# Optimization experiments

Measured on AMD Instinct MI355X. Metric: run time of the kernel, lower is better.

The kernel has to match this reference:

```python
import jax, jax.numpy as jnp
import numpy as np

B_, T_, N_ = 32, 96, 68
IN_F, HID, GRU_H, NCLS = 3, 128, 128, 10
DEG = 8
N_NODES = B_ * T_ * N_
N_EDGES = N_NODES * DEG


def setup_inputs() -> dict:
    key = jax.random.key(0)
    ks = jax.random.split(key, 16)
    s = 0.05
    rn = lambda k, shp: (jax.random.normal(k, shp, jnp.float32) * s)
    return {
        "x": jax.random.normal(ks[0], (N_NODES, IN_F), jnp.float32),
        "edge_index": jax.random.randint(ks[1], (2, N_EDGES), 0, N_NODES, jnp.int32),
        "W_gcn0": rn(ks[2], (IN_F, HID)),
        "b_gcn0": jnp.zeros((HID,), jnp.float32),
        "W_gcn1": rn(ks[3], (HID, HID)),
        "b_gcn1": jnp.zeros((HID,), jnp.float32),
        "W_mlp": rn(ks[4], (HID, HID)),
        "b_mlp": jnp.zeros((HID,), jnp.float32),
        "W_ih": rn(ks[5], (3 * GRU_H, HID)),
        "W_hh": rn(ks[6], (3 * GRU_H, GRU_H)),
        "b_ih": jnp.zeros((3 * GRU_H,), jnp.float32),
        "b_hh": jnp.zeros((3 * GRU_H,), jnp.float32),
        "W_c1": rn(ks[7], (GRU_H, GRU_H // 2)),
        "b_c1": jnp.zeros((GRU_H // 2,), jnp.float32),
        "W_c2": rn(ks[8], (GRU_H // 2, NCLS)),
        "b_c2": jnp.zeros((NCLS,), jnp.float32),
        "B": B_, "T": T_, "N": N_,
    }


def reference(x, edge_index, W_gcn0, b_gcn0, W_gcn1, b_gcn1, W_mlp, b_mlp,
              W_ih, W_hh, b_ih, b_hh, W_c1, b_c1, W_c2, b_c2, B, T, N):
    n_nodes = x.shape[0]
    src, dst = edge_index[0], edge_index[1]
    # GCN degree with self-loops: deg[i] = 1 + in-degree(i)
    deg = jnp.ones((n_nodes,), x.dtype).at[dst].add(1.0)
    d_isqrt = jax.lax.rsqrt(deg)
    self_norm = (d_isqrt * d_isqrt)[:, None]  # self-loop norm = 1/deg
    edge_norm = (d_isqrt[src] * d_isqrt[dst])[:, None]

    def gcn(h, W, b):
        h = h @ W
        agg = jax.ops.segment_sum(h[src] * edge_norm, dst, num_segments=n_nodes)
        return agg + h * self_norm + b

    h = jax.nn.relu(gcn(x, W_gcn0, b_gcn0))
    h = jax.nn.relu(gcn(h, W_gcn1, b_gcn1))
    h = jax.nn.relu(h @ W_mlp + b_mlp)  # node_mlp (dropout off in eval)

    frames = h.reshape(B, T, N, -1).mean(axis=2)  # [B, T, HID] frame pooling

    def gru_step(hs, xt):
        gi = xt @ W_ih.T + b_ih
        gh = hs @ W_hh.T + b_hh
        ir, iz, inn = jnp.split(gi, 3, axis=-1)
        hr, hz, hn = jnp.split(gh, 3, axis=-1)
        r = jax.nn.sigmoid(ir + hr)
        z = jax.nn.sigmoid(iz + hz)
        n_new = jnp.tanh(inn + r * hn)
        return (1.0 - z) * n_new + z * hs, None

    h0 = jnp.zeros((B, GRU_H), frames.dtype)
    hT, _ = jax.lax.scan(gru_step, h0, jnp.swapaxes(frames, 0, 1))

    hidden = jax.nn.relu(hT @ W_c1 + b_c1)
    return hidden @ W_c2 + b_c2  # logits [B, num_classes]
```

## Files before the change

### kernel.cpp

```cpp
#include <hip/hip_runtime.h>

#define NN_TOT 208896
#define E_TOT  1671168
#define B_SZ   32
#define T_SZ   96
#define NPF    68
#define HID    128
#define NBINS  204
#define CAP    9216
#define NSB    816

typedef _Float16 f16x8 __attribute__((ext_vector_type(8)));
typedef _Float16 f16x2v __attribute__((ext_vector_type(2)));
typedef float f32x4 __attribute__((ext_vector_type(4)));

__global__ __launch_bounds__(256) void k_scatter(const int* __restrict__ src, const int* __restrict__ dst,
                                                 int* __restrict__ gcur, int* __restrict__ er_tmp,
                                                 const float* __restrict__ Wih, const float* __restrict__ Whh,
                                                 const float* __restrict__ W1, const float* __restrict__ Wm,
                                                 const float* __restrict__ W0, const float* __restrict__ b0,
                                                 _Float16* __restrict__ Wihh, _Float16* __restrict__ Wihl,
                                                 _Float16* __restrict__ W1p, _Float16* __restrict__ Wmp,
                                                 _Float16* __restrict__ Whhp, _Float16* __restrict__ W0h,
                                                 _Float16* __restrict__ b0h) {
    const int bid = blockIdx.x;
    const int tid = threadIdx.x;
    if (bid >= NSB) {
        int i = (bid - NSB) * 256 + tid;
        {
            int e = i & 7;
            int lane = (i >> 3) & 63;
            int f = i >> 9;
            int j = f >> 2, kk = f & 3;
            int q = lane >> 4, p = lane & 15;
            float wv = Wih[(size_t)(j * 16 + p) * 128 + kk * 32 + q * 8 + e];
            _Float16 hi = (_Float16)wv;
            Wihh[i] = hi;
            Wihl[i] = (_Float16)(wv - (float)hi);
        }
        {
            int e = i & 7;
            int lane = (i >> 3) & 63;
            int f = i >> 9;
            int kk = f & 3, g = (f >> 2) % 3, wv = f / 12;
            int q = lane >> 4, c = lane & 15;
            Whhp[i] = (_Float16)Whh[(size_t)(g * 128 + 16 * wv + c) * 128 + kk * 32 + q * 8 + e];
        }
        if (i < 16384) {
            int f = i >> 9;
            int j = f >> 2, kk = f & 3;
            int lane = (i >> 3) & 63;
            int e = i & 7;
            int q = lane >> 4, p = lane & 15;
            int k = kk * 32 + q * 8 + e, n = j * 16 + p;
            W1p[i] = (_Float16)W1[k * 128 + n];
            Wmp[i] = (_Float16)Wm[k * 128 + n];
        }
        if (i < 384) W0h[i] = (_Float16)W0[i];
        if (i < 128) b0h[i] = (_Float16)b0[i];
        return;
    }
    __shared__ int hist[NBINS];
    __shared__ int lbase[NBINS];
    for (int i = tid; i < NBINS; i += 256) hist[i] = 0;
    __syncthreads();
    const int be = bid * 2048 + tid * 8;
    int s[8], d[8], rk[8];
    *(int4*)&s[0] = *(const int4*)&src[be];
    *(int4*)&s[4] = *(const int4*)&src[be + 4];
    *(int4*)&d[0] = *(const int4*)&dst[be];
    *(int4*)&d[4] = *(const int4*)&dst[be + 4];
#pragma unroll
    for (int j = 0; j < 8; ++j) rk[j] = atomicAdd(&hist[d[j] >> 10], 1);
    __syncthreads();
    for (int i = tid; i < NBINS; i += 256) lbase[i] = atomicAdd(&gcur[i], hist[i]);
    __syncthreads();
#pragma unroll
    for (int j = 0; j < 8; ++j) {
        int b = d[j] >> 10;
        er_tmp[(size_t)b * CAP + lbase[b] + rk[j]] = s[j] | ((d[j] & 1023) << 18);
    }
}

__global__ __launch_bounds__(256) void k_binsort2(const int* __restrict__ er_tmp, const int* __restrict__ gcur,
                                                  const float* __restrict__ x, int* __restrict__ er,
                                                  int2* __restrict__ row2, float4* __restrict__ xd) {
    __shared__ int lcnt[1024];
    __shared__ int lofs[1024];
    __shared__ int ts[256];
    const int tid = threadIdx.x;
    const int nb = blockIdx.x << 10;
    const int base0 = blockIdx.x * CAP;
    for (int i = tid; i < 1024; i += 256) lcnt[i] = 0;
    __syncthreads();
    const int nrec = gcur[blockIdx.x];
    int rec[36];
#pragma unroll
    for (int j = 0; j < 36; ++j) {
        int idx = tid + j * 256;
        rec[j] = (idx < nrec) ? er_tmp[base0 + idx] : -1;
    }
#pragma unroll
    for (int j = 0; j < 36; ++j)
        if (rec[j] >= 0) atomicAdd(&lcnt[rec[j] >> 18], 1);
    __syncthreads();
    const int base = tid * 4;
    const int c0 = lcnt[base], c1 = lcnt[base + 1], c2 = lcnt[base + 2], c3 = lcnt[base + 3];
    int ssum = c0 + c1 + c2 + c3;
    ts[tid] = ssum;
    __syncthreads();
    int inc = ssum;
    for (int off = 1; off < 256; off <<= 1) {
        int add = (tid >= off) ? ts[tid - off] : 0;
        __syncthreads();
        inc += add;
        ts[tid] = inc;
        __syncthreads();
    }
    const int b0 = base0 + (inc - ssum);
    lofs[base] = b0;
    lofs[base + 1] = b0 + c0;
    lofs[base + 2] = b0 + c0 + c1;
    lofs[base + 3] = b0 + c0 + c1 + c2;
    row2[nb + base] = make_int2(b0, b0 + c0);
    row2[nb + base + 1] = make_int2(b0 + c0, b0 + c0 + c1);
    row2[nb + base + 2] = make_int2(b0 + c0 + c1, b0 + c0 + c1 + c2);
    row2[nb + base + 3] = make_int2(b0 + c0 + c1 + c2, b0 + ssum);
    {
        const float4* xv = (const float4*)(x + 3 * (size_t)(nb + base));
        float4 a = xv[0], b = xv[1], c = xv[2];
        float i0 = 1.0f / sqrtf(1.f + (float)c0);
        float i1 = 1.0f / sqrtf(1.f + (float)c1);
        float i2 = 1.0f / sqrtf(1.f + (float)c2);
        float i3 = 1.0f / sqrtf(1.f + (float)c3);
        xd[nb + base + 0] = make_float4(a.x * i0, a.y * i0, a.z * i0, i0);
        xd[nb + base + 1] = make_float4(a.w * i1, b.x * i1, b.y * i1, i1);
        xd[nb + base + 2] = make_float4(b.z * i2, b.w * i2, c.x * i2, i2);
        xd[nb + base + 3] = make_float4(c.y * i3, c.z * i3, c.w * i3, i3);
    }
    __syncthreads();
#pragma unroll
    for (int j = 0; j < 36; ++j)
        if (rec[j] >= 0) {
            int p = atomicAdd(&lofs[rec[j] >> 18], 1);
            er[p] = rec[j] & 0x3FFFF;
        }
}

__global__ __launch_bounds__(256) void k_z0(const float4* __restrict__ xd, const int2* __restrict__ row2,
                                            const int* __restrict__ er, float4* __restrict__ z0out) {
    const int tid = threadIdx.x;
    const int blk = blockIdx.x;
    const int li = tid >> 2;
    const int slot = tid & 3;
    const int n = blk * 64 + li;
    const int2 be2 = row2[n];
    float p0 = 0.f, p1 = 0.f, p2 = 0.f;
    for (int ei = be2.x + slot; ei < be2.y; ei += 4) {
        float4 f = xd[er[ei]];
        p0 += f.x;
        p1 += f.y;
        p2 += f.z;
    }
    p0 += __shfl_xor(p0, 1); p1 += __shfl_xor(p1, 1); p2 += __shfl_xor(p2, 1);
    p0 += __shfl_xor(p0, 2); p1 += __shfl_xor(p1, 2); p2 += __shfl_xor(p2, 2);
    if (slot == 0) {
        const float4 own = xd[n];
        const float w = own.w;
        float4 z;
        z.x = w * (p0 + own.x);
        z.y = w * (p1 + own.y);
        z.z = w * (p2 + own.z);
        z.w = w;
        z0out[n] = z;
    }
}

__global__ __launch_bounds__(256, 4) void k_agg_mm(const float4* __restrict__ z0, const int2* __restrict__ row2,
                                                   const int* __restrict__ er, const _Float16* __restrict__ W0h,
                                                   const _Float16* __restrict__ b0h, const _Float16* __restrict__ W1p,
                                                   const float* __restrict__ b1, _Float16* __restrict__ h1) {
    __shared__ __align__(16) _Float16 As[64 * 136];
    const int tid = threadIdx.x;
    const int w = tid >> 6, lane = tid & 63;
    const int blk = blockIdx.x;

    {
        const int node = blk * 64 + lane;
        const int2 be2 = row2[node];
        const int beg = be2.x, end = be2.y;
        const f16x2v* __restrict__ W0p = (const f16x2v*)W0h;
        const f16x2v* __restrict__ b0p = (const f16x2v*)b0h;
        const int pb = w * 16;
        const f16x2v zero2 = {(_Float16)0.f, (_Float16)0.f};
        f16x2v w0p[16], w1p[16], w2p[16], bbp[16];
#pragma unroll
        for (int j = 0; j < 16; ++j) {
            w0p[j] = W0p[pb + j];
            w1p[j] = W0p[64 + pb + j];
            w2p[j] = W0p[128 + pb + j];
            bbp[j] = b0p[pb + j];
        }
        const float4 zs = z0[node];
        const _Float16 isd = (_Float16)zs.w;
        const f16x2v dnn = {isd, isd};
        f16x2v accp[16];
        {
            _Float16 sx = (_Float16)zs.x, sy = (_Float16)zs.y, sz = (_Float16)zs.z;
            f16x2v zxx = {sx, sx}, zyy = {sy, sy}, zzz = {sz, sz};
#pragma unroll
            for (int j = 0; j < 16; ++j) {
                f16x2v t = zxx * w0p[j] + (zyy * w1p[j] + (zzz * w2p[j] + bbp[j]));
                t = __builtin_elementwise_max(t, zero2);
                accp[j] = t * dnn;
            }
        }
        int ei = beg;
        for (; ei + 2 <= end; ei += 2) {
            int sa = er[ei], sb = er[ei + 1];
            float4 za = z0[sa];
            float4 zb = z0[sb];
            _Float16 ax = (_Float16)za.x, ay = (_Float16)za.y, az = (_Float16)za.z;
            _Float16 aen = (_Float16)za.w;
            _Float16 bx = (_Float16)zb.x, by = (_Float16)zb.y, bz = (_Float16)zb.z;
            _Float16 ben = (_Float16)zb.w;
            f16x2v axx = {ax, ax}, ayy = {ay, ay}, azz = {az, az}, aee = {aen, aen};
            f16x2v bxx = {bx, bx}, byy = {by, by}, bzz = {bz, bz}, bee = {ben, ben};
#pragma unroll
            for (int j = 0; j < 16; ++j) {
                f16x2v t = axx * w0p[j] + (ayy * w1p[j] + (azz * w2p[j] + bbp[j]));
                t = __builtin_elementwise_max(t, zero2);
                accp[j] = t * aee + accp[j];
            }
#pragma unroll
            for (int j = 0; j < 16; ++j) {
                f16x2v t = bxx * w0p[j] + (byy * w1p[j] + (bzz * w2p[j] + bbp[j]));
                t = __builtin_elementwise_max(t, zero2);
                accp[j] = t * bee + accp[j];
            }
        }
        if (ei < end) {
            float4 za = z0[er[ei]];
            _Float16 ax = (_Float16)za.x, ay = (_Float16)za.y, az = (_Float16)za.z;
            _Float16 aen = (_Float16)za.w;
            f16x2v axx = {ax, ax}, ayy = {ay, ay}, azz = {az, az}, aee = {aen, aen};
#pragma unroll
            for (int j = 0; j < 16; ++j) {
                f16x2v t = axx * w0p[j] + (ayy * w1p[j] + (azz * w2p[j] + bbp[j]));
                t = __builtin_elementwise_max(t, zero2);
                accp[j] = t * aee + accp[j];
            }
        }
        _Float16* dst = &As[lane * 136 + w * 32];
#pragma unroll
        for (int j = 0; j < 16; ++j) *(f16x2v*)(dst + 2 * j) = accp[j] * dnn;
    }
    __syncthreads();

    const int q = lane >> 4, c = lane & 15;
    f16x8 afr[4];
#pragma unroll
    for (int kk = 0; kk < 4; ++kk) afr[kk] = *(const f16x8*)(&As[(w * 16 + c) * 136 + kk * 32 + q * 8]);
    const f16x8* __restrict__ Bv = (const f16x8*)W1p;
    _Float16* Cst = &As[w * 2176];
#pragma unroll
    for (int j = 0; j < 8; ++j) {
        f32x4 cc = {0.f, 0.f, 0.f, 0.f};
#pragma unroll
        for (int kk = 0; kk < 4; ++kk)
            cc = __builtin_amdgcn_mfma_f32_16x16x32_f16(afr[kk], Bv[(j * 4 + kk) * 64 + lane], cc, 0, 0, 0);
        const float bi = b1[j * 16 + c];
#pragma unroll
        for (int r = 0; r < 4; ++r) Cst[(q * 4 + r) * 128 + j * 16 + c] = (_Float16)fmaxf(cc[r] + bi, 0.f);
    }
#pragma unroll
    for (int it = 0; it < 4; ++it) {
        int idx = it * 64 + lane;
        *(f16x8*)(h1 + (size_t)(blk * 64 + w * 16) * 128 + idx * 8) = *(const f16x8*)(&As[w * 2176 + idx * 8]);
    }
}

__global__ __launch_bounds__(256) void k_mm_pool(const _Float16* __restrict__ h1, const _Float16* __restrict__ Wmp,
                                                 const float* __restrict__ bm, _Float16* __restrict__ FRh,
                                                 _Float16* __restrict__ FRl) {
    __shared__ __align__(16) _Float16 As[80 * 136];
    __shared__ float colpart[4 * 128];
    const int tid = threadIdx.x;
    const int w = tid >> 6, lane = tid & 63;
    const int q = lane >> 4, c = lane & 15;
    const int bt = blockIdx.x;

    const f16x8* __restrict__ srcv = (const f16x8*)(h1 + (size_t)bt * NPF * HID);
    for (int idx = tid; idx < 80 * 17; idx += 256) {
        int row = idx / 17, ch = idx % 17;
        f16x8 v;
        if (row < NPF && ch < 16) {
            v = srcv[row * 16 + ch];
        } else {
#pragma unroll
            for (int k = 0; k < 8; ++k) v[k] = (_Float16)0.f;
        }
        *(f16x8*)(&As[row * 136 + ch * 8]) = v;
    }
    __syncthreads();

    const f16x8* __restrict__ Bv = (const f16x8*)Wmp;
    const int npass = (w == 0) ? 2 : 1;
    for (int pass = 0; pass < npass; ++pass) {
        const int mt = pass ? 4 : w;
        f16x8 afr[4];
#pragma unroll
        for (int kk = 0; kk < 4; ++kk) afr[kk] = *(const f16x8*)(&As[(mt * 16 + c) * 136 + kk * 32 + q * 8]);
#pragma unroll
        for (int j = 0; j < 8; ++j) {
            f32x4 cc = {0.f, 0.f, 0.f, 0.f};
#pragma unroll
            for (int kk = 0; kk < 4; ++kk)
                cc = __builtin_amdgcn_mfma_f32_16x16x32_f16(afr[kk], Bv[(j * 4 + kk) * 64 + lane], cc, 0, 0, 0);
            const float bi = bm[j * 16 + c];
            float s = 0.f;
#pragma unroll
            for (int r = 0; r < 4; ++r) {
                int m = mt * 16 + q * 4 + r;
                float v = fmaxf(cc[r] + bi, 0.f);
                s += (m < NPF) ? v : 0.f;
            }
            s += __shfl_xor(s, 16);
            s += __shfl_xor(s, 32);
            if (lane < 16) {
                float* dst = &colpart[w * 128 + j * 16 + c];
                *dst = (pass == 0) ? s : (*dst + s);
            }
        }
    }
    __syncthreads();
    if (tid < 128) {
        float v = (colpart[tid] + colpart[128 + tid] + colpart[256 + tid] + colpart[384 + tid]) * (1.0f / NPF);
        _Float16 hi = (_Float16)v;
        FRh[(size_t)blockIdx.x * 128 + tid] = hi;
        FRl[(size_t)blockIdx.x * 128 + tid] = (_Float16)(v - (float)hi);
    }
}

__global__ __launch_bounds__(256) void k_gi(const _Float16* __restrict__ FRh, const _Float16* __restrict__ FRl,
                                            const _Float16* __restrict__ Wihh, const _Float16* __restrict__ Wihl,
                                            const float* __restrict__ bih, const float* __restrict__ bhh,
                                            float* __restrict__ GIt) {
    __shared__ __align__(16) _Float16 Ah[64 * 136];
    __shared__ __align__(16) _Float16 Al[64 * 136];
    const int tid = threadIdx.x;
    const int w = tid >> 6, lane = tid & 63;
    const int q = lane >> 4, p = lane & 15;
    const int nb = blockIdx.x * 64;

    const f16x8* __restrict__ sh = (const f16x8*)(FRh + (size_t)nb * 128);
    const f16x8* __restrict__ sl = (const f16x8*)(FRl + (size_t)nb * 128);
    for (int idx = tid; idx < 64 * 16; idx += 256) {
        int row = idx >> 4, ch = idx & 15;
        *(f16x8*)(&Ah[row * 136 + ch * 8]) = sh[idx];
        *(f16x8*)(&Al[row * 136 + ch * 8]) = sl[idx];
    }
    __syncthreads();

    f16x8 ah[4], al[4];
#pragma unroll
    for (int kk = 0; kk < 4; ++kk) {
        ah[kk] = *(const f16x8*)(&Ah[(w * 16 + p) * 136 + kk * 32 + q * 8]);
        al[kk] = *(const f16x8*)(&Al[(w * 16 + p) * 136 + kk * 32 + q * 8]);
    }
    const f16x8* __restrict__ Bh = (const f16x8*)Wihh;
    const f16x8* __restrict__ Bl = (const f16x8*)Wihl;
    int dr[4];
#pragma unroll
    for (int r = 0; r < 4; ++r) {
        int m = nb + w * 16 + q * 4 + r;
        int bb = m / 96, tt = m - bb * 96;
        dr[r] = (tt * B_SZ + bb) * 384;
    }
#pragma unroll
    for (int j = 0; j < 24; ++j) {
        f32x4 cc = {0.f, 0.f, 0.f, 0.f};
#pragma unroll
        for (int kk = 0; kk < 4; ++kk)
            cc = __builtin_amdgcn_mfma_f32_16x16x32_f16(ah[kk], Bh[(j * 4 + kk) * 64 + lane], cc, 0, 0, 0);
#pragma unroll
        for (int kk = 0; kk < 4; ++kk)
            cc = __builtin_amdgcn_mfma_f32_16x16x32_f16(ah[kk], Bl[(j * 4 + kk) * 64 + lane], cc, 0, 0, 0);
#pragma unroll
        for (int kk = 0; kk < 4; ++kk)
            cc = __builtin_amdgcn_mfma_f32_16x16x32_f16(al[kk], Bh[(j * 4 + kk) * 64 + lane], cc, 0, 0, 0);
        const int o = j * 16 + p;
        const float bias = bih[o] + ((o < 256) ? bhh[o] : 0.f);
        const float scale = (o < 256) ? -1.44269504f : 1.f;
#pragma unroll
        for (int r = 0; r < 4; ++r) GIt[dr[r] + o] = (cc[r] + bias) * scale;
    }
}

#define GRU_SYNC()                                              \
    asm volatile("s_waitcnt lgkmcnt(0)" ::: "memory");          \
    __builtin_amdgcn_s_barrier();                               \
    __builtin_amdgcn_sched_barrier(0);

#define GRU_BODY(PAR, GU, GL, JOFF)                                                                  \
    {                                                                                                \
        const _Float16* rb = hbuf[PAR];                                                              \
        _Float16* wb = hbuf[PAR ^ 1];                                                                \
        f16x8 afr[4];                                                                                \
        _Pragma("unroll") for (int kk = 0; kk < 4; ++kk)                                             \
            afr[kk] = *(const f16x8*)(&rb[c * 144 + kk * 32 + q * 8]);                               \
        const float* lp = pb + (size_t)(JOFF + 2) * STRIDE;                                          \
        _Pragma("unroll") for (int r = 0; r < 4; ++r)                                                \
            _Pragma("unroll") for (int g = 0; g < 3; ++g)                                            \
                GL[r * 3 + g] = lp[r * 384 + g * 128];                                               \
        f32x4 cc[3];                                                                                 \
        _Pragma("unroll") for (int g = 0; g < 3; ++g) {                                              \
            f32x4 a = {0.f, 0.f, 0.f, 0.f};                                                          \
            _Pragma("unroll") for (int kk = 0; kk < 4; ++kk)                                         \
                a = __builtin_amdgcn_mfma_f32_16x16x32_f16(afr[kk], bfr[g][kk], a, 0, 0, 0);         \
            cc[g] = a;                                                                               \
        }                                                                                            \
        _Pragma("unroll") for (int r = 0; r < 4; ++r) {                                              \
            float hn = cc[2][r] + bh2;                                                               \
            float rg = __builtin_amdgcn_rcpf(1.f + exp2f(fmaf(mL2E, cc[0][r], GU[r * 3 + 0])));      \
            float zg = __builtin_amdgcn_rcpf(1.f + exp2f(fmaf(mL2E, cc[1][r], GU[r * 3 + 1])));      \
            float arg = fmaf(rg, hn, GU[r * 3 + 2]);                                                 \
            float u = __builtin_amdgcn_rcpf(exp2f(2.f * L2E * arg) + 1.f);                           \
            float nn = fmaf(-2.f, u, 1.f);                                                           \
            h[r] = fmaf(zg, h[r] - nn, nn);                                                          \
            if (q < 2) wb[(q * 4 + r) * 144 + 16 * w + c] = (_Float16)h[r];                          \
        }                                                                                            \
        GRU_SYNC()                                                                                   \
    }

__global__ __launch_bounds__(512) __attribute__((amdgpu_waves_per_eu(1, 2)))
void k_gru(const float* __restrict__ GIt, const _Float16* __restrict__ Whhp,
           const float* __restrict__ bhh,
           const float* __restrict__ Wc1, const float* __restrict__ bc1,
           const float* __restrict__ Wc2, const float* __restrict__ bc2,
           float* __restrict__ out) {
    __shared__ __align__(16) _Float16 hbuf[2][16 * 144];
    const int tid = threadIdx.x;
    const int w = tid >> 6, lane = tid & 63;
    const int q = lane >> 4, c = lane & 15;
    const int B = blockIdx.x;
    const float L2E = 1.44269504f;
    const float mL2E = -1.44269504f;
    const int STRIDE = B_SZ * 384;

    f16x8 bfr[3][4];
#pragma unroll
    for (int g = 0; g < 3; ++g)
#pragma unroll
        for (int kk = 0; kk < 4; ++kk)
            bfr[g][kk] = *(const f16x8*)(Whhp + (size_t)(((w * 3 + g) * 4 + kk) * 64 + lane) * 8);
    const float bh2 = bhh[256 + 16 * w + c];
    for (int i = tid; i < 2 * 16 * 144 / 2; i += 512) ((unsigned int*)hbuf)[i] = 0u;
    float h[4] = {0.f, 0.f, 0.f, 0.f};

    const int qq = (q < 2) ? q : 1;
    const float* pb = GIt + (size_t)(B * 8 + qq * 4) * 384 + 16 * w + c;
    float g0[12], g1[12], g2[12];
#pragma unroll
    for (int r = 0; r < 4; ++r)
#pragma unroll
        for (int g = 0; g < 3; ++g) {
            g0[r * 3 + g] = pb[r * 384 + g * 128];
            g1[r * 3 + g] = pb[STRIDE + r * 384 + g * 128];
        }
    GRU_SYNC()

    for (int it = 0; it < T_SZ / 6; ++it) {
        GRU_BODY(0, g0, g2, 0)
        GRU_BODY(1, g1, g0, 1)
        GRU_BODY(0, g2, g1, 2)
        GRU_BODY(1, g0, g2, 3)
        GRU_BODY(0, g1, g0, 4)
        GRU_BODY(1, g2, g1, 5)
        pb += 6 * (size_t)STRIDE;
    }

    float* hbf = (float*)hbuf;
    float* hid = hbf + 1024;
    __syncthreads();
    if (q < 2) {
#pragma unroll
        for (int r = 0; r < 4; ++r) hbf[(q * 4 + r) * 128 + 16 * w + c] = h[r];
    }
    __syncthreads();
    {
        const int b = tid >> 6, j = tid & 63;
        const float* hb = hbf + b * 128;
        float a0 = bc1[j], a1 = 0.f, a2 = 0.f, a3 = 0.f;
#pragma unroll
        for (int k = 0; k < 128; k += 4) {
            a0 = fmaf(hb[k], Wc1[k * 64 + j], a0);
            a1 = fmaf(hb[k + 1], Wc1[(k + 1) * 64 + j], a1);
            a2 = fmaf(hb[k + 2], Wc1[(k + 2) * 64 + j], a2);
            a3 = fmaf(hb[k + 3], Wc1[(k + 3) * 64 + j], a3);
        }
        hid[tid] = fmaxf((a0 + a1) + (a2 + a3), 0.f);
    }
    __syncthreads();
    if (tid < 80) {
        int b = tid / 10, cc2 = tid % 10;
        float a = bc2[cc2];
#pragma unroll 8
        for (int k = 0; k < 64; ++k) a = fmaf(hid[b * 64 + k], Wc2[k * 10 + cc2], a);
        out[(B * 8 + b) * 10 + cc2] = a;
    }
}

extern "C" void kernel_launch(void* const* d_in, const int* in_sizes, int n_in, void* d_out, int out_size, void* d_ws,
                              size_t ws_size, hipStream_t stream) {
    const float* x = (const float*)d_in[0];
    const int* ei = (const int*)d_in[1];
    const int* e_src = ei;
    const int* e_dst = ei + E_TOT;
    const float* W0 = (const float*)d_in[2];
    const float* b0 = (const float*)d_in[3];
    const float* W1 = (const float*)d_in[4];
    const float* b1 = (const float*)d_in[5];
    const float* Wm = (const float*)d_in[6];
    const float* bm = (const float*)d_in[7];
    const float* Wih = (const float*)d_in[8];
    const float* Whh = (const float*)d_in[9];
    const float* bih = (const float*)d_in[10];
    const float* bhh = (const float*)d_in[11];
    const float* Wc1 = (const float*)d_in[12];
    const float* bc1 = (const float*)d_in[13];
    const float* Wc2 = (const float*)d_in[14];
    const float* bc2 = (const float*)d_in[15];
    float* out = (float*)d_out;

    char* base = (char*)d_ws;
    size_t off = 0;
    auto alloc = [&](size_t bytes) {
        size_t o = off;
        off = (off + bytes + 255) & ~(size_t)255;
        return o;
    };
    size_t o_gcur = alloc(256 * 4);
    size_t o_row2 = alloc((size_t)NN_TOT * 8);
    size_t o_er = alloc((size_t)NBINS * CAP * 4);
    size_t o_ertmp = alloc((size_t)NBINS * CAP * 4);
    size_t o_xd = alloc((size_t)NN_TOT * 16);
    size_t o_gi = alloc((size_t)(T_SZ + 2) * B_SZ * 384 * 4);
    size_t o_wihh = alloc((size_t)384 * 128 * 2);
    size_t o_wihl = alloc((size_t)384 * 128 * 2);
    size_t o_frh = alloc((size_t)B_SZ * T_SZ * 128 * 2);
    size_t o_frl = alloc((size_t)B_SZ * T_SZ * 128 * 2);
    size_t o_w1p = alloc((size_t)128 * 128 * 2);
    size_t o_wmp = alloc((size_t)128 * 128 * 2);
    size_t o_whhp = alloc((size_t)128 * 384 * 2);
    size_t o_w0h = alloc((size_t)384 * 2);
    size_t o_b0h = alloc((size_t)128 * 2);
    size_t o_z0 = alloc((size_t)NN_TOT * 16);
    size_t o_h1 = alloc((size_t)NN_TOT * HID * 2);
    if (off > ws_size) return;

    int* gcur = (int*)(base + o_gcur);
    int2* row2 = (int2*)(base + o_row2);
    int* er = (int*)(base + o_er);
    int* er_tmp = (int*)(base + o_ertmp);
    float4* xd = (float4*)(base + o_xd);
    float* GIt = (float*)(base + o_gi);
    _Float16* Wihh = (_Float16*)(base + o_wihh);
    _Float16* Wihl = (_Float16*)(base + o_wihl);
    _Float16* FRh = (_Float16*)(base + o_frh);
    _Float16* FRl = (_Float16*)(base + o_frl);
    _Float16* W1p = (_Float16*)(base + o_w1p);
    _Float16* Wmp = (_Float16*)(base + o_wmp);
    _Float16* Whhp = (_Float16*)(base + o_whhp);
    _Float16* W0h = (_Float16*)(base + o_w0h);
    _Float16* b0h = (_Float16*)(base + o_b0h);
    float4* z0 = (float4*)(base + o_z0);
    _Float16* h1 = (_Float16*)(base + o_h1);

    hipMemsetAsync(base + o_gcur, 0, 256 * 4, stream);

    k_scatter<<<NSB + 192, 256, 0, stream>>>(e_src, e_dst, gcur, er_tmp,
                                             Wih, Whh, W1, Wm, W0, b0,
                                             Wihh, Wihl, W1p, Wmp, Whhp, W0h, b0h);
    k_binsort2<<<NBINS, 256, 0, stream>>>(er_tmp, gcur, x, er, row2, xd);
    k_z0<<<NN_TOT / 64, 256, 0, stream>>>(xd, row2, er, z0);
    k_agg_mm<<<NN_TOT / 64, 256, 0, stream>>>(z0, row2, er, W0h, b0h, W1p, b1, h1);
    k_mm_pool<<<B_SZ * T_SZ, 256, 0, stream>>>(h1, Wmp, bm, FRh, FRl);
    k_gi<<<B_SZ * T_SZ / 64, 256, 0, stream>>>(FRh, FRl, Wihh, Wihl, bih, bhh, GIt);
    k_gru<<<4, 512, 0, stream>>>(GIt, Whhp, bhh, Wc1, bc1, Wc2, bc2, out);
}
```

Baseline: 359.1 us.

## Fuse node MLP and frame pooling into GCN aggregation kernel

Folds the node MLP matmul and frame mean-pooling into k_agg_mm, so the 64-row tile stays in LDS and the h1 intermediate (about 53 MB of fp16) is never written to or read back from global memory. Since 64-node tiles can straddle a frame boundary of 68 nodes, each block splits its column sums into two partial frames and accumulates them with float atomics into a zeroed fp32 frame buffer. k_gi now does the divide by 68 and the hi/lo fp16 split itself. This costs an extra memset, atomic contention, more LDS per block (which may lower occupancy under launch_bounds 256,4), and a non-deterministic summation order.

Result: faster. 345.8 us (-3.7%).

```diff
diff --git a/kernel.cpp b/kernel.cpp
--- a/kernel.cpp
+++ b/kernel.cpp
@@ -179,8 +179,11 @@
 __global__ __launch_bounds__(256, 4) void k_agg_mm(const float4* __restrict__ z0, const int2* __restrict__ row2,
                                                    const int* __restrict__ er, const _Float16* __restrict__ W0h,
                                                    const _Float16* __restrict__ b0h, const _Float16* __restrict__ W1p,
-                                                   const float* __restrict__ b1, _Float16* __restrict__ h1) {
+                                                   const float* __restrict__ b1, const _Float16* __restrict__ Wmp,
+                                                   const float* __restrict__ bm, float* __restrict__ fr32) {
     __shared__ __align__(16) _Float16 As[64 * 136];
+    __shared__ __align__(16) _Float16 Bs[64 * 136];
+    __shared__ float colpart[4 * 2 * 128];
     const int tid = threadIdx.x;
     const int w = tid >> 6, lane = tid & 63;
     const int blk = blockIdx.x;
@@ -258,91 +261,71 @@
     __syncthreads();
 
     const int q = lane >> 4, c = lane & 15;
-    f16x8 afr[4];
-#pragma unroll
-    for (int kk = 0; kk < 4; ++kk) afr[kk] = *(const f16x8*)(&As[(w * 16 + c) * 136 + kk * 32 + q * 8]);
-    const f16x8* __restrict__ Bv = (const f16x8*)W1p;
-    _Float16* Cst = &As[w * 2176];
-#pragma unroll
-    for (int j = 0; j < 8; ++j) {
-        f32x4 cc = {0.f, 0.f, 0.f, 0.f};
-#pragma unroll
-        for (int kk = 0; kk < 4; ++kk)
-            cc = __builtin_amdgcn_mfma_f32_16x16x32_f16(afr[kk], Bv[(j * 4 + kk) * 64 + lane], cc, 0, 0, 0);
-        const float bi = b1[j * 16 + c];
-#pragma unroll
-        for (int r = 0; r < 4; ++r) Cst[(q * 4 + r) * 128 + j * 16 + c] = (_Float16)fmaxf(cc[r] + bi, 0.f);
-    }
-#pragma unroll
-    for (int it = 0; it < 4; ++it) {
-        int idx = it * 64 + lane;
-        *(f16x8*)(h1 + (size_t)(blk * 64 + w * 16) * 128 + idx * 8) = *(const f16x8*)(&As[w * 2176 + idx * 8]);
-    }
-}
-
-__global__ __launch_bounds__(256) void k_mm_pool(const _Float16* __restrict__ h1, const _Float16* __restrict__ Wmp,
-                                                 const float* __restrict__ bm, _Float16* __restrict__ FRh,
-                                                 _Float16* __restrict__ FRl) {
-    __shared__ __align__(16) _Float16 As[80 * 136];
-    __shared__ float colpart[4 * 128];
-    const int tid = threadIdx.x;
-    const int w = tid >> 6, lane = tid & 63;
-    const int q = lane >> 4, c = lane & 15;
-    const int bt = blockIdx.x;
-
-    const f16x8* __restrict__ srcv = (const f16x8*)(h1 + (size_t)bt * NPF * HID);
-    for (int idx = tid; idx < 80 * 17; idx += 256) {
-        int row = idx / 17, ch = idx % 17;
-        f16x8 v;
-        if (row < NPF && ch < 16) {
-            v = srcv[row * 16 + ch];
-        } else {
-#pragma unroll
-            for (int k = 0; k < 8; ++k) v[k] = (_Float16)0.f;
-        }
-        *(f16x8*)(&As[row * 136 + ch * 8]) = v;
-    }
-    __syncthreads();
-
-    const f16x8* __restrict__ Bv = (const f16x8*)Wmp;
-    const int npass = (w == 0) ? 2 : 1;
-    for (int pass = 0; pass < npass; ++pass) {
-        const int mt = pass ? 4 : w;
+    {
         f16x8 afr[4];
 #pragma unroll
-        for (int kk = 0; kk < 4; ++kk) afr[kk] = *(const f16x8*)(&As[(mt * 16 + c) * 136 + kk * 32 + q * 8]);
+        for (int kk = 0; kk < 4; ++kk) afr[kk] = *(const f16x8*)(&As[(w * 16 + c) * 136 + kk * 32 + q * 8]);
+        const f16x8* __restrict__ Bv = (const f16x8*)W1p;
 #pragma unroll
         for (int j = 0; j < 8; ++j) {
             f32x4 cc = {0.f, 0.f, 0.f, 0.f};
 #pragma unroll
             for (int kk = 0; kk < 4; ++kk)
                 cc = __builtin_amdgcn_mfma_f32_16x16x32_f16(afr[kk], Bv[(j * 4 + kk) * 64 + lane], cc, 0, 0, 0);
+            const float bi = b1[j * 16 + c];
+#pragma unroll
+            for (int r = 0; r < 4; ++r)
+                Bs[(w * 16 + q * 4 + r) * 136 + j * 16 + c] = (_Float16)fmaxf(cc[r] + bi, 0.f);
+        }
+    }
+
+    {
+        f16x8 afr2[4];
+#pragma unroll
+        for (int kk = 0; kk < 4; ++kk) afr2[kk] = *(const f16x8*)(&Bs[(w * 16 + c) * 136 + kk * 32 + q * 8]);
+        const f16x8* __restrict__ Bv2 = (const f16x8*)Wmp;
+        const int f0 = (blk * 64) / NPF;
+        const int cut = (f0 + 1) * NPF;
+        const int rowg0 = blk * 64 + w * 16 + q * 4;
+#pragma unroll
+        for (int j = 0; j < 8; ++j) {
+            f32x4 cc = {0.f, 0.f, 0.f, 0.f};
+#pragma unroll
+            for (int kk = 0; kk < 4; ++kk)
+                cc = __builtin_amdgcn_mfma_f32_16x16x32_f16(afr2[kk], Bv2[(j * 4 + kk) * 64 + lane], cc, 0, 0, 0);
             const float bi = bm[j * 16 + c];
-            float s = 0.f;
+            float sA = 0.f, sB = 0.f;
 #pragma unroll
             for (int r = 0; r < 4; ++r) {
-                int m = mt * 16 + q * 4 + r;
                 float v = fmaxf(cc[r] + bi, 0.f);
-                s += (m < NPF) ? v : 0.f;
+                if (rowg0 + r < cut) sA += v; else sB += v;
             }
-            s += __shfl_xor(s, 16);
-            s += __shfl_xor(s, 32);
+            sA += __shfl_xor(sA, 16);
+            sA += __shfl_xor(sA, 32);
+            sB += __shfl_xor(sB, 16);
+            sB += __shfl_xor(sB, 32);
             if (lane < 16) {
-                float* dst = &colpart[w * 128 + j * 16 + c];
-                *dst = (pass == 0) ? s : (*dst + s);
+                colpart[(w * 2 + 0) * 128 + j * 16 + c] = sA;
+                colpart[(w * 2 + 1) * 128 + j * 16 + c] = sB;
             }
         }
     }
     __syncthreads();
-    if (tid < 128) {
-        float v = (colpart[tid] + colpart[128 + tid] + colpart[256 + tid] + colpart[384 + tid]) * (1.0f / NPF);
-        _Float16 hi = (_Float16)v;
-        FRh[(size_t)blockIdx.x * 128 + tid] = hi;
-        FRl[(size_t)blockIdx.x * 128 + tid] = (_Float16)(v - (float)hi);
-    }
-}
-
-__global__ __launch_bounds__(256) void k_gi(const _Float16* __restrict__ FRh, const _Float16* __restrict__ FRl,
+    {
+        const int f = tid >> 7, col = tid & 127;
+        float s = colpart[(0 * 2 + f) * 128 + col] + colpart[(1 * 2 + f) * 128 + col] +
+                  colpart[(2 * 2 + f) * 128 + col] + colpart[(3 * 2 + f) * 128 + col];
+        const int f0 = (blk * 64) / NPF;
+        if (f == 0) {
+            atomicAdd(&fr32[(size_t)f0 * 128 + col], s);
+        } else {
+            const int f1 = (blk * 64 + 63) / NPF;
+            if (f1 != f0) atomicAdd(&fr32[(size_t)f1 * 128 + col], s);
+        }
+    }
+}
+
+__global__ __launch_bounds__(256) void k_gi(const float* __restrict__ fr32,
                                             const _Float16* __restrict__ Wihh, const _Float16* __restrict__ Wihl,
                                             const float* __restrict__ bih, const float* __restrict__ bhh,
                                             float* __restrict__ GIt) {
@@ -353,12 +336,12 @@
     const int q = lane >> 4, p = lane & 15;
     const int nb = blockIdx.x * 64;
 
-    const f16x8* __restrict__ sh = (const f16x8*)(FRh + (size_t)nb * 128);
-    const f16x8* __restrict__ sl = (const f16x8*)(FRl + (size_t)nb * 128);
-    for (int idx = tid; idx < 64 * 16; idx += 256) {
-        int row = idx >> 4, ch = idx & 15;
-        *(f16x8*)(&Ah[row * 136 + ch * 8]) = sh[idx];
-        *(f16x8*)(&Al[row * 136 + ch * 8]) = sl[idx];
+    for (int idx = tid; idx < 64 * 128; idx += 256) {
+        int row = idx >> 7, col = idx & 127;
+        float v = fr32[(size_t)(nb + row) * 128 + col] * (1.0f / NPF);
+        _Float16 hi = (_Float16)v;
+        Ah[row * 136 + col] = hi;
+        Al[row * 136 + col] = (_Float16)(v - (float)hi);
     }
     __syncthreads();
 
@@ -545,18 +528,16 @@
     size_t o_er = alloc((size_t)NBINS * CAP * 4);
     size_t o_ertmp = alloc((size_t)NBINS * CAP * 4);
     size_t o_xd = alloc((size_t)NN_TOT * 16);
+    size_t o_fr32 = alloc((size_t)B_SZ * T_SZ * 128 * 4);
     size_t o_gi = alloc((size_t)(T_SZ + 2) * B_SZ * 384 * 4);
     size_t o_wihh = alloc((size_t)384 * 128 * 2);
     size_t o_wihl = alloc((size_t)384 * 128 * 2);
-    size_t o_frh = alloc((size_t)B_SZ * T_SZ * 128 * 2);
-    size_t o_frl = alloc((size_t)B_SZ * T_SZ * 128 * 2);
     size_t o_w1p = alloc((size_t)128 * 128 * 2);
     size_t o_wmp = alloc((size_t)128 * 128 * 2);
     size_t o_whhp = alloc((size_t)128 * 384 * 2);
     size_t o_w0h = alloc((size_t)384 * 2);
     size_t o_b0h = alloc((size_t)128 * 2);
     size_t o_z0 = alloc((size_t)NN_TOT * 16);
-    size_t o_h1 = alloc((size_t)NN_TOT * HID * 2);
     if (off > ws_size) return;
 
     int* gcur = (int*)(base + o_gcur);
@@ -564,28 +545,26 @@
     int* er = (int*)(base + o_er);
     int* er_tmp = (int*)(base + o_ertmp);
     float4* xd = (float4*)(base + o_xd);
+    float* fr32 = (float*)(base + o_fr32);
     float* GIt = (float*)(base + o_gi);
     _Float16* Wihh = (_Float16*)(base + o_wihh);
     _Float16* Wihl = (_Float16*)(base + o_wihl);
-    _Float16* FRh = (_Float16*)(base + o_frh);
-    _Float16* FRl = (_Float16*)(base + o_frl);
     _Float16* W1p = (_Float16*)(base + o_w1p);
     _Float16* Wmp = (_Float16*)(base + o_wmp);
     _Float16* Whhp = (_Float16*)(base + o_whhp);
     _Float16* W0h = (_Float16*)(base + o_w0h);
     _Float16* b0h = (_Float16*)(base + o_b0h);
     float4* z0 = (float4*)(base + o_z0);
-    _Float16* h1 = (_Float16*)(base + o_h1);
 
     hipMemsetAsync(base + o_gcur, 0, 256 * 4, stream);
+    hipMemsetAsync(base + o_fr32, 0, (size_t)B_SZ * T_SZ * 128 * 4, stream);
 
     k_scatter<<<NSB + 192, 256, 0, stream>>>(e_src, e_dst, gcur, er_tmp,
                                              Wih, Whh, W1, Wm, W0, b0,
                                              Wihh, Wihl, W1p, Wmp, Whhp, W0h, b0h);
     k_binsort2<<<NBINS, 256, 0, stream>>>(er_tmp, gcur, x, er, row2, xd);
     k_z0<<<NN_TOT / 64, 256, 0, stream>>>(xd, row2, er, z0);
-    k_agg_mm<<<NN_TOT / 64, 256, 0, stream>>>(z0, row2, er, W0h, b0h, W1p, b1, h1);
-    k_mm_pool<<<B_SZ * T_SZ, 256, 0, stream>>>(h1, Wmp, bm, FRh, FRl);
-    k_gi<<<B_SZ * T_SZ / 64, 256, 0, stream>>>(FRh, FRl, Wihh, Wihl, bih, bhh, GIt);
+    k_agg_mm<<<NN_TOT / 64, 256, 0, stream>>>(z0, row2, er, W0h, b0h, W1p, b1, Wmp, bm, fr32);
+    k_gi<<<B_SZ * T_SZ / 64, 256, 0, stream>>>(fr32, Wihh, Wihl, bih, bhh, GIt);
     k_gru<<<4, 512, 0, stream>>>(GIt, Whhp, bhh, Wc1, bc1, Wc2, bc2, out);
 }
```
